# Kernel tuning notes

Measured on AMD Instinct MI355X. Metric: run time of the kernel, lower is better.

The kernel has to match this reference:

```python
import math
import jax, jax.numpy as jnp
import numpy as np

B, S, D = 4, 2048, 1024
EPS_LN = 1e-5
EPS_MAS = 1e-9


def layernorm(x, g, b):
    m = jnp.mean(x, axis=-1, keepdims=True)
    v = jnp.mean(jnp.square(x - m), axis=-1, keepdims=True)
    return (x - m) * jax.lax.rsqrt(v + EPS_LN) * g + b


def spl(x, proto_w, mu_w, mu_b, gate):
    # match_values = x @ proto^T / sqrt(d);  comp = silu(x @ mu^T + b)
    match = jnp.einsum('bsd,od->bso', x, proto_w) / math.sqrt(x.shape[-1])
    comp = jax.nn.silu(jnp.einsum('bsd,od->bso', x, mu_w) + mu_b)
    return comp, match, gate


def branch(comp, match, gate, passthrough):
    # mas_normalize on the 1-D gate vector (cost), broadcast over [B,S,D]
    cost = gate / (jnp.max(jnp.abs(gate)) + EPS_MAS)
    rl = match - cost
    mrl = jax.nn.relu(rl)
    mask = (rl > 0).astype(comp.dtype)
    return comp * mrl + passthrough * (1.0 - mask)


def causal_attention(q, k, v):
    # num_heads = 1, head_dim = D, is_causal=True
    scale = 1.0 / math.sqrt(q.shape[-1])
    scores = jnp.einsum('bqd,bkd->bqk', q, k) * scale
    causal = jnp.tril(jnp.ones((q.shape[1], k.shape[1]), dtype=bool))
    scores = jnp.where(causal, scores, jnp.asarray(-1e9, scores.dtype))
    p = jax.nn.softmax(scores, axis=-1)
    return jnp.einsum('bqk,bkd->bqd', p, v)


def setup_inputs() -> dict:
    key = jax.random.key(0)
    ks = jax.random.split(key, 16)
    d = D
    std = 0.02
    inp = {
        'x': jax.random.normal(ks[0], (B, S, d), jnp.float32),
        'ln_g': jnp.ones((d,), jnp.float32),
        'ln_b': jnp.zeros((d,), jnp.float32),
    }
    names = ['q', 'k', 'v', 'o']
    for i, n in enumerate(names):
        inp[f'{n}_mu_w'] = std * jax.random.normal(ks[1 + 3 * i], (d, d), jnp.float32)
        inp[f'{n}_mu_b'] = jnp.zeros((d,), jnp.float32)
        inp[f'{n}_proto'] = std * jax.random.normal(ks[2 + 3 * i], (d, d), jnp.float32)
        inp[f'{n}_gate'] = 0.1 * jax.random.normal(ks[3 + 3 * i], (d,), jnp.float32)
    return inp


def reference(x, ln_g, ln_b,
              q_mu_w, q_mu_b, q_proto, q_gate,
              k_mu_w, k_mu_b, k_proto, k_gate,
              v_mu_w, v_mu_b, v_proto, v_gate,
              o_mu_w, o_mu_b, o_proto, o_gate):
    ln1_out = layernorm(x, ln_g, ln_b)

    c_q, mv_q, g_q = spl(ln1_out, q_proto, q_mu_w, q_mu_b, q_gate)
    c_k, mv_k, g_k = spl(ln1_out, k_proto, k_mu_w, k_mu_b, k_gate)
    c_v, mv_v, g_v = spl(ln1_out, v_proto, v_mu_w, v_mu_b, v_gate)

    q = branch(c_q, mv_q, g_q, ln1_out)
    k = branch(c_k, mv_k, g_k, ln1_out)
    v = branch(c_v, mv_v, g_v, ln1_out)

    attn_out = causal_attention(q, k, v)

    c_o, mv_o, g_o = spl(attn_out, o_proto, o_mu_w, o_mu_b, o_gate)
    masked_o = branch(c_o, mv_o, g_o, attn_out)

    x_out = x + masked_o
    return x_out
```

## Files before the change

kernel.cpp:

```cpp
#include <hip/hip_runtime.h>
#include <hip/hip_bf16.h>
#include <cmath>
#include <cstdint>

typedef _Float16 f16;
typedef _Float16 f16x8 __attribute__((ext_vector_type(8)));
typedef float f32x4 __attribute__((ext_vector_type(4)));

#define D_ 1024
#define S_ 2048


__device__ __forceinline__ void gload_lds16(const void* g, void* l) {
  __builtin_amdgcn_global_load_lds(
      (const __attribute__((address_space(1))) void*)(unsigned long long)(uintptr_t)g,
      (__attribute__((address_space(3))) void*)(unsigned int)(uintptr_t)l,
      16, 0, 0);
}

__device__ __forceinline__ int lds_off(int row, int cb) {
  return (row << 5) + ((cb ^ ((row >> 1) & 3)) << 3);
}

__device__ __forceinline__ void split1024(float v, f16& h, f16& l) {
  float s = v * 1024.f;
  h = (f16)s;
  l = (f16)(s - (float)h);
}

__device__ __forceinline__ void stage_tile(const f16* __restrict__ src, int ld,
                                           f16* lds, int wid, int lane) {
  const int r = (wid << 5) + (lane >> 2);
  const int c = (lane & 3) ^ ((r >> 1) & 3);
  const f16* g0 = src + (size_t)r * ld + (c << 3);
  gload_lds16(g0, lds + (wid << 10));
  gload_lds16(g0 + (size_t)(ld << 4), lds + (wid << 10) + 512);
}

__global__ __launch_bounds__(256) void convert_w(
    const float* __restrict__ s0, const float* __restrict__ s1,
    const float* __restrict__ s2, const float* __restrict__ s3,
    const float* __restrict__ s4, const float* __restrict__ s5,
    const float* __restrict__ s6, const float* __restrict__ s7,
    f16* __restrict__ dst) {
  const float* srcs[8] = {s0, s1, s2, s3, s4, s5, s6, s7};
  const float* sp = srcs[blockIdx.y];
  f16* hi = dst + (size_t)blockIdx.y * 2097152;
  f16* lo = hi + 1048576;
  const int i = (blockIdx.x * 256 + threadIdx.x) << 2;
  float4 f = *(const float4*)(sp + i);
  __align__(8) f16 h4[4], l4[4];
  split1024(f.x, h4[0], l4[0]); split1024(f.y, h4[1], l4[1]);
  split1024(f.z, h4[2], l4[2]); split1024(f.w, h4[3], l4[3]);
  *(uint2*)(hi + i) = *(uint2*)h4;
  *(uint2*)(lo + i) = *(uint2*)l4;
}

__global__ __launch_bounds__(256) void cost_k(
    const float* __restrict__ g0, const float* __restrict__ g1,
    const float* __restrict__ g2, const float* __restrict__ g3,
    float* __restrict__ cost) {
  const float* gp = blockIdx.x == 0 ? g0 : blockIdx.x == 1 ? g1
                   : blockIdx.x == 2 ? g2 : g3;
  const int t = threadIdx.x;
  float4 v = *(const float4*)(gp + (t << 2));
  float mx = fmaxf(fmaxf(fabsf(v.x), fabsf(v.y)), fmaxf(fabsf(v.z), fabsf(v.w)));
  for (int o = 32; o; o >>= 1) mx = fmaxf(mx, __shfl_xor(mx, o, 64));
  __shared__ float red[4];
  if ((t & 63) == 0) red[t >> 6] = mx;
  __syncthreads();
  mx = fmaxf(fmaxf(red[0], red[1]), fmaxf(red[2], red[3]));
  const float den = mx + 1e-9f;
  float4 o = {v.x / den, v.y / den, v.z / den, v.w / den};
  *(float4*)(cost + (blockIdx.x << 10) + (t << 2)) = o;
}

__global__ __launch_bounds__(256) void layernorm_k(
    const float* __restrict__ x, const float* __restrict__ g,
    const float* __restrict__ bta, f16* __restrict__ Lh, f16* __restrict__ Ll) {
  const int row = blockIdx.x, t = threadIdx.x;
  const float* xr = x + (size_t)row * D_;
  float4 v = *(const float4*)(xr + (t << 2));
  float s = v.x + v.y + v.z + v.w;
  float q = v.x * v.x + v.y * v.y + v.z * v.z + v.w * v.w;
  for (int o = 32; o; o >>= 1) { s += __shfl_xor(s, o, 64); q += __shfl_xor(q, o, 64); }
  __shared__ float red[8];
  const int wid = t >> 6;
  if ((t & 63) == 0) { red[wid] = s; red[4 + wid] = q; }
  __syncthreads();
  s = red[0] + red[1] + red[2] + red[3];
  q = red[4] + red[5] + red[6] + red[7];
  const float mean = s * (1.f / D_);
  const float var = q * (1.f / D_) - mean * mean;
  const float inv = 1.f / sqrtf(var + 1e-5f);
  float4 gv = *(const float4*)(g + (t << 2));
  float4 bv = *(const float4*)(bta + (t << 2));
  __align__(8) f16 h4[4], l4[4];
  split1024((v.x - mean) * inv * gv.x + bv.x, h4[0], l4[0]);
  split1024((v.y - mean) * inv * gv.y + bv.y, h4[1], l4[1]);
  split1024((v.z - mean) * inv * gv.z + bv.z, h4[2], l4[2]);
  split1024((v.w - mean) * inv * gv.w + bv.w, h4[3], l4[3]);
  const size_t off = (size_t)row * D_ + (t << 2);
  *(uint2*)(Lh + off) = *(uint2*)h4;
  *(uint2*)(Ll + off) = *(uint2*)l4;
}

template <int EPI, int MUP>
__global__ __launch_bounds__(512, 1) void dual_gemm_v2(
    const f16* __restrict__ Ah, const f16* __restrict__ Al,
    const f16* __restrict__ Wph, const f16* __restrict__ Wpl,
    const f16* __restrict__ Wmh, const f16* __restrict__ Wml,
    const float* __restrict__ bias, const float* __restrict__ cost,
    const f16* __restrict__ passh, const f16* __restrict__ passl,
    const float* __restrict__ xres, f16* __restrict__ outh,
    f16* __restrict__ outl, float* __restrict__ outf) {
  __shared__ __align__(16) f16 smem[65536];
  const int tid = threadIdx.x, wid = tid >> 6, lane = tid & 63;
  const int row0 = blockIdx.x << 8, col0 = blockIdx.y << 7;
  const int wr = (wid >> 1) << 6, wc = (wid & 1) << 6;
  const int arow = lane & 15, cbk = lane >> 4;

  const int sr = tid >> 2;
  const int sc = ((tid & 3) ^ ((sr >> 1) & 3)) << 3;
  const int wbase = wid << 9;

  const f16* pA0 = Ah + (size_t)(row0 + sr) * D_ + sc;
  const f16* pA1 = Ah + (size_t)(row0 + 128 + sr) * D_ + sc;
  const f16* pL0 = Al + (size_t)(row0 + sr) * D_ + sc;
  const f16* pL1 = Al + (size_t)(row0 + 128 + sr) * D_ + sc;
  const f16* pPh = Wph + (size_t)(col0 + sr) * D_ + sc;
  const f16* pPl = Wpl + (size_t)(col0 + sr) * D_ + sc;
  const f16* pMh = Wmh + (size_t)(col0 + sr) * D_ + sc;
  const f16* pMl = Wml + (size_t)(col0 + sr) * D_ + sc;

  const f32x4 zero = {0.f, 0.f, 0.f, 0.f};
  f32x4 accP[4][4], accM[4][4];
#pragma unroll
  for (int m = 0; m < 4; ++m)
#pragma unroll
    for (int n = 0; n < 4; ++n) { accP[m][n] = zero; accM[m][n] = zero; }

  auto STAGE = [&](f16* buf, int k) {
    gload_lds16(pA0 + k, buf + wbase);
    gload_lds16(pA1 + k, buf + 4096 + wbase);
    gload_lds16(pL0 + k, buf + 8192 + wbase);
    gload_lds16(pL1 + k, buf + 12288 + wbase);
    gload_lds16(pPh + k, buf + 16384 + wbase);
    gload_lds16(pPl + k, buf + 20480 + wbase);
    gload_lds16(pMh + k, buf + 24576 + wbase);
    gload_lds16(pMl + k, buf + 28672 + wbase);
  };

  auto COMPUTE = [&](const f16* buf) {
    const f16* bAh = buf;
    const f16* bAl = buf + 8192;
    const f16* bPh = buf + 16384;
    const f16* bPl = buf + 20480;
    const f16* bMh = buf + 24576;
    const f16* bMl = buf + 28672;
    f16x8 ah[4], al[4];
#pragma unroll
    for (int m = 0; m < 4; ++m) {
      const int ao = lds_off(wr + m * 16 + arow, cbk);
      ah[m] = *(const f16x8*)&bAh[ao];
      al[m] = *(const f16x8*)&bAl[ao];
    }
#pragma unroll
    for (int n = 0; n < 4; ++n) {
      const int bo = lds_off(wc + n * 16 + arow, cbk);
      f16x8 bph = *(const f16x8*)&bPh[bo];
      f16x8 bpl = *(const f16x8*)&bPl[bo];
      f16x8 bmh = *(const f16x8*)&bMh[bo];
      f16x8 bml = *(const f16x8*)&bMl[bo];
#pragma unroll
      for (int m = 0; m < 4; ++m) {
        accP[m][n] = __builtin_amdgcn_mfma_f32_16x16x32_f16(ah[m], bph, accP[m][n], 0, 0, 0);
        accP[m][n] = __builtin_amdgcn_mfma_f32_16x16x32_f16(ah[m], bpl, accP[m][n], 0, 0, 0);
        accP[m][n] = __builtin_amdgcn_mfma_f32_16x16x32_f16(al[m], bph, accP[m][n], 0, 0, 0);
        accM[m][n] = __builtin_amdgcn_mfma_f32_16x16x32_f16(ah[m], bmh, accM[m][n], 0, 0, 0);
        accM[m][n] = __builtin_amdgcn_mfma_f32_16x16x32_f16(ah[m], bml, accM[m][n], 0, 0, 0);
        if (MUP == 3)
          accM[m][n] = __builtin_amdgcn_mfma_f32_16x16x32_f16(al[m], bmh, accM[m][n], 0, 0, 0);
      }
    }
  };

  STAGE(smem, 0);
  int cur = 0;
  for (int t = 0; t < 31; ++t) {
    STAGE(smem + ((cur ^ 1) << 15), (t + 1) << 5);
    asm volatile("s_waitcnt vmcnt(8)\n\ts_barrier" ::: "memory");
    __builtin_amdgcn_s_setprio(1);
    COMPUTE(smem + (cur << 15));
    __builtin_amdgcn_s_setprio(0);
    asm volatile("s_waitcnt lgkmcnt(0)\n\ts_barrier" ::: "memory");
    cur ^= 1;
  }
  asm volatile("s_waitcnt vmcnt(0)\n\ts_barrier" ::: "memory");
  __builtin_amdgcn_s_setprio(1);
  COMPUTE(smem + (cur << 15));
  __builtin_amdgcn_s_setprio(0);

#pragma unroll
  for (int m = 0; m < 4; ++m) {
    const int rb = row0 + wr + m * 16 + ((lane >> 4) << 2);
#pragma unroll
    for (int n = 0; n < 4; ++n) {
      const int col = col0 + wc + n * 16 + (lane & 15);
      const float cb2 = cost[col], bb = bias[col];
#pragma unroll
      for (int j = 0; j < 4; ++j) {
        const size_t off = (size_t)(rb + j) * D_ + col;
        const float match = accP[m][n][j] * (1.f / 33554432.f);
        const float pre = accM[m][n][j] * (1.f / 1048576.f) + bb;
        const float comp = pre / (1.f + expf(-pre));
        const float rl = match - cb2;
        float ov;
        if (rl > 0.f) ov = comp * rl;
        else ov = ((float)passh[off] + (float)passl[off]) * (1.f / 1024.f);
        if (EPI == 0) {
          f16 h, l; split1024(ov, h, l);
          outh[off] = h; outl[off] = l;
        } else {
          outf[off] = xres[off] + ov;
        }
      }
    }
  }
}

__global__ __launch_bounds__(256) void transpose_v(
    const f16* __restrict__ Vh, const f16* __restrict__ Vl,
    f16* __restrict__ VTh, f16* __restrict__ VTl) {
  const int iz = blockIdx.z, b = iz & 3;
  const f16* src = (iz >> 2) ? Vl : Vh;
  f16* dst = (iz >> 2) ? VTl : VTh;
  const int d0 = blockIdx.x << 6, s0 = blockIdx.y << 6;
  __shared__ f16 tl[64][65];
  const int c = threadIdx.x & 63, r4 = threadIdx.x >> 6;
  const f16* vb = src + (size_t)b * S_ * D_;
#pragma unroll
  for (int i = 0; i < 16; ++i) {
    const int sr = (r4 << 4) + i;
    tl[sr][c] = vb[(size_t)(s0 + sr) * D_ + d0 + c];
  }
  __syncthreads();
  f16* db = dst + (size_t)b * D_ * S_;
#pragma unroll
  for (int i = 0; i < 16; ++i) {
    const int dr = (r4 << 4) + i;
    db[(size_t)(d0 + dr) * S_ + s0 + c] = tl[c][dr];
  }
}

__global__ __launch_bounds__(256, 2) void scores_gemm(
    const f16* __restrict__ Qh, const f16* __restrict__ Ql,
    const f16* __restrict__ Kh, const f16* __restrict__ Kl,
    float* __restrict__ SC) {
  const int rt = blockIdx.x, ct = blockIdx.y, b = blockIdx.z;
  if (ct > rt) return;
  __shared__ __align__(16) f16 lQh[4096], lQl[4096], lKh[4096], lKl[4096];
  const int tid = threadIdx.x, wid = tid >> 6, lane = tid & 63;
  const int row0 = rt << 7, col0 = ct << 7;
  const int wr = (wid >> 1) << 6, wc = (wid & 1) << 6;
  const int arow = lane & 15, cb = lane >> 4;
  const f32x4 zero = {0.f, 0.f, 0.f, 0.f};
  f32x4 acc[4][4];
#pragma unroll
  for (int m = 0; m < 4; ++m)
#pragma unroll
    for (int n = 0; n < 4; ++n) acc[m][n] = zero;
  const f16* Qhb = Qh + ((size_t)b * S_ + row0) * D_;
  const f16* Qlb = Ql + ((size_t)b * S_ + row0) * D_;
  const f16* Khb = Kh + ((size_t)b * S_ + col0) * D_;
  const f16* Klb = Kl + ((size_t)b * S_ + col0) * D_;
  for (int k = 0; k < D_; k += 32) {
    stage_tile(Qhb + k, D_, lQh, wid, lane);
    stage_tile(Qlb + k, D_, lQl, wid, lane);
    stage_tile(Khb + k, D_, lKh, wid, lane);
    stage_tile(Klb + k, D_, lKl, wid, lane);
    __syncthreads();
    f16x8 bh[4], bl[4];
#pragma unroll
    for (int n = 0; n < 4; ++n) {
      const int bo = lds_off(wc + n * 16 + arow, cb);
      bh[n] = *(const f16x8*)&lKh[bo];
      bl[n] = *(const f16x8*)&lKl[bo];
    }
#pragma unroll
    for (int m = 0; m < 4; ++m) {
      const int ao = lds_off(wr + m * 16 + arow, cb);
      f16x8 ah = *(const f16x8*)&lQh[ao];
      f16x8 al = *(const f16x8*)&lQl[ao];
#pragma unroll
      for (int n = 0; n < 4; ++n) {
        acc[m][n] = __builtin_amdgcn_mfma_f32_16x16x32_f16(ah, bh[n], acc[m][n], 0, 0, 0);
        acc[m][n] = __builtin_amdgcn_mfma_f32_16x16x32_f16(ah, bl[n], acc[m][n], 0, 0, 0);
        acc[m][n] = __builtin_amdgcn_mfma_f32_16x16x32_f16(al, bh[n], acc[m][n], 0, 0, 0);
      }
    }
    __syncthreads();
  }
  float* scb = SC + (size_t)b * S_ * S_;
#pragma unroll
  for (int m = 0; m < 4; ++m) {
    const int rb = row0 + wr + m * 16 + ((lane >> 4) << 2);
#pragma unroll
    for (int n = 0; n < 4; ++n) {
      const int col = col0 + wc + n * 16 + (lane & 15);
#pragma unroll
      for (int j = 0; j < 4; ++j)
        scb[(size_t)(rb + j) * S_ + col] = acc[m][n][j] * (1.f / 33554432.f);
    }
  }
}

__global__ __launch_bounds__(256) void softmax_rows(float* __restrict__ SC) {
  const int r = blockIdx.x;
  const int s = r & 2047;
  float* rowf = SC + (size_t)r * S_;
  const int t = threadIdx.x, c0 = t << 3;
  float f[8];
  float4 u0 = *(const float4*)(rowf + c0);
  float4 u1 = *(const float4*)(rowf + c0 + 4);
  f[0] = u0.x; f[1] = u0.y; f[2] = u0.z; f[3] = u0.w;
  f[4] = u1.x; f[5] = u1.y; f[6] = u1.z; f[7] = u1.w;
  float mx = -3.0e38f;
#pragma unroll
  for (int j = 0; j < 8; ++j)
    if (c0 + j <= s) mx = fmaxf(mx, f[j]);
  for (int o = 32; o; o >>= 1) mx = fmaxf(mx, __shfl_xor(mx, o, 64));
  __shared__ float red[8];
  const int wid = t >> 6;
  if ((t & 63) == 0) red[wid] = mx;
  __syncthreads();
  mx = fmaxf(fmaxf(red[0], red[1]), fmaxf(red[2], red[3]));
  float e[8];
  float sum = 0.f;
#pragma unroll
  for (int j = 0; j < 8; ++j) {
    e[j] = (c0 + j <= s) ? expf(f[j] - mx) : 0.f;
    sum += e[j];
  }
  for (int o = 32; o; o >>= 1) sum += __shfl_xor(sum, o, 64);
  if ((t & 63) == 0) red[4 + wid] = sum;
  __syncthreads();
  sum = red[4] + red[5] + red[6] + red[7];
  f16* rowh = (f16*)rowf;
  __align__(16) f16 ph[8], pl[8];
#pragma unroll
  for (int j = 0; j < 8; ++j) {
    float p = (e[j] / sum) * 2048.f;
    ph[j] = (f16)p;
    pl[j] = (f16)(p - (float)ph[j]);
  }
  *(uint4*)(rowh + c0) = *(uint4*)ph;
  *(uint4*)(rowh + 2048 + c0) = *(uint4*)pl;
}

__global__ __launch_bounds__(256, 2) void pv_gemm(
    const f16* __restrict__ P, const f16* __restrict__ VTh,
    const f16* __restrict__ VTl, f16* __restrict__ Ath, f16* __restrict__ Atl) {
  const int rt = blockIdx.x, ct = blockIdx.y, b = blockIdx.z;
  __shared__ __align__(16) f16 lPh[4096], lPl[4096], lVh[4096], lVl[4096];
  const int tid = threadIdx.x, wid = tid >> 6, lane = tid & 63;
  const int row0 = rt << 7, col0 = ct << 7;
  const int wr = (wid >> 1) << 6, wc = (wid & 1) << 6;
  const int arow = lane & 15, cb = lane >> 4;
  const f32x4 zero = {0.f, 0.f, 0.f, 0.f};
  f32x4 acc[4][4];
#pragma unroll
  for (int m = 0; m < 4; ++m)
#pragma unroll
    for (int n = 0; n < 4; ++n) acc[m][n] = zero;
  const f16* Pb = P + ((size_t)b * S_ + row0) * 4096;
  const f16* Vhb = VTh + (size_t)b * D_ * S_ + (size_t)col0 * S_;
  const f16* Vlb = VTl + (size_t)b * D_ * S_ + (size_t)col0 * S_;
  const int kend = (rt + 1) << 7;
  for (int k = 0; k < kend; k += 32) {
    stage_tile(Pb + k, 4096, lPh, wid, lane);
    stage_tile(Pb + 2048 + k, 4096, lPl, wid, lane);
    stage_tile(Vhb + k, S_, lVh, wid, lane);
    stage_tile(Vlb + k, S_, lVl, wid, lane);
    __syncthreads();
    f16x8 bh[4], bl[4];
#pragma unroll
    for (int n = 0; n < 4; ++n) {
      const int bo = lds_off(wc + n * 16 + arow, cb);
      bh[n] = *(const f16x8*)&lVh[bo];
      bl[n] = *(const f16x8*)&lVl[bo];
    }
#pragma unroll
    for (int m = 0; m < 4; ++m) {
      const int ao = lds_off(wr + m * 16 + arow, cb);
      f16x8 ah = *(const f16x8*)&lPh[ao];
      f16x8 al = *(const f16x8*)&lPl[ao];
#pragma unroll
      for (int n = 0; n < 4; ++n) {
        acc[m][n] = __builtin_amdgcn_mfma_f32_16x16x32_f16(ah, bh[n], acc[m][n], 0, 0, 0);
        acc[m][n] = __builtin_amdgcn_mfma_f32_16x16x32_f16(ah, bl[n], acc[m][n], 0, 0, 0);
        acc[m][n] = __builtin_amdgcn_mfma_f32_16x16x32_f16(al, bh[n], acc[m][n], 0, 0, 0);
      }
    }
    __syncthreads();
  }
#pragma unroll
  for (int m = 0; m < 4; ++m) {
    const int rb = row0 + wr + m * 16 + ((lane >> 4) << 2);
#pragma unroll
    for (int n = 0; n < 4; ++n) {
      const int col = col0 + wc + n * 16 + (lane & 15);
#pragma unroll
      for (int j = 0; j < 4; ++j) {
        const float at = acc[m][n][j] * (1.f / 2097152.f);
        const size_t off = ((size_t)b * S_ + rb + j) * D_ + col;
        f16 h, l; split1024(at, h, l);
        Ath[off] = h; Atl[off] = l;
      }
    }
  }
}

extern "C" void kernel_launch(void* const* d_in, const int* in_sizes, int n_in,
                              void* d_out, int out_size, void* d_ws, size_t ws_size,
                              hipStream_t stream) {
  (void)in_sizes; (void)n_in; (void)out_size; (void)ws_size;
  const float* x      = (const float*)d_in[0];
  const float* ln_g   = (const float*)d_in[1];
  const float* ln_b   = (const float*)d_in[2];
  const float* q_mu_w = (const float*)d_in[3];
  const float* q_mu_b = (const float*)d_in[4];
  const float* q_pro  = (const float*)d_in[5];
  const float* q_gate = (const float*)d_in[6];
  const float* k_mu_w = (const float*)d_in[7];
  const float* k_mu_b = (const float*)d_in[8];
  const float* k_pro  = (const float*)d_in[9];
  const float* k_gate = (const float*)d_in[10];
  const float* v_mu_w = (const float*)d_in[11];
  const float* v_mu_b = (const float*)d_in[12];
  const float* v_pro  = (const float*)d_in[13];
  const float* v_gate = (const float*)d_in[14];
  const float* o_mu_w = (const float*)d_in[15];
  const float* o_mu_b = (const float*)d_in[16];
  const float* o_pro  = (const float*)d_in[17];
  const float* o_gate = (const float*)d_in[18];

  char* w = (char*)d_ws;
  f16* WB = (f16*)w;
  const size_t WS = 2097152;
  f16* Lh  = (f16*)(w + 33554432);
  f16* Ll  = (f16*)(w + 50331648);
  f16* Qh  = (f16*)(w + 67108864);
  f16* Ql  = (f16*)(w + 83886080);
  f16* Kh  = (f16*)(w + 100663296);
  f16* Kl  = (f16*)(w + 117440512);
  f16* VTh = (f16*)(w + 134217728);
  f16* VTl = (f16*)(w + 150994944);
  float* SC = (float*)(w + 167772160);
  float* COST = (float*)(w + 234881024);
  f16* Vh = (f16*)SC;
  f16* Vl = (f16*)(w + 184549376);
  f16* Ath = Qh;  f16* Atl = Ql;

  convert_w<<<dim3(1024, 8), 256, 0, stream>>>(
      q_pro, q_mu_w, k_pro, k_mu_w, v_pro, v_mu_w, o_pro, o_mu_w, WB);
  cost_k<<<4, 256, 0, stream>>>(q_gate, k_gate, v_gate, o_gate, COST);
  layernorm_k<<<8192, 256, 0, stream>>>(x, ln_g, ln_b, Lh, Ll);

  dual_gemm_v2<0, 3><<<dim3(32, 8), 512, 0, stream>>>(
      Lh, Ll, WB, WB + 1048576, WB + WS, WB + WS + 1048576,
      q_mu_b, COST, Lh, Ll, nullptr, Qh, Ql, nullptr);
  dual_gemm_v2<0, 3><<<dim3(32, 8), 512, 0, stream>>>(
      Lh, Ll, WB + 2 * WS, WB + 2 * WS + 1048576, WB + 3 * WS, WB + 3 * WS + 1048576,
      k_mu_b, COST + 1024, Lh, Ll, nullptr, Kh, Kl, nullptr);
  dual_gemm_v2<0, 3><<<dim3(32, 8), 512, 0, stream>>>(
      Lh, Ll, WB + 4 * WS, WB + 4 * WS + 1048576, WB + 5 * WS, WB + 5 * WS + 1048576,
      v_mu_b, COST + 2048, Lh, Ll, nullptr, Vh, Vl, nullptr);

  transpose_v<<<dim3(16, 32, 8), 256, 0, stream>>>(Vh, Vl, VTh, VTl);
  scores_gemm<<<dim3(16, 16, 4), 256, 0, stream>>>(Qh, Ql, Kh, Kl, SC);
  softmax_rows<<<8192, 256, 0, stream>>>(SC);
  pv_gemm<<<dim3(16, 8, 4), 256, 0, stream>>>((const f16*)SC, VTh, VTl, Ath, Atl);

  dual_gemm_v2<1, 2><<<dim3(32, 8), 512, 0, stream>>>(
      Ath, Atl, WB + 6 * WS, WB + 6 * WS + 1048576, WB + 7 * WS, WB + 7 * WS + 1048576,
      o_mu_b, COST + 3072, Ath, Atl, x, nullptr, nullptr, (float*)d_out);
}
```

Measured before the change: 712.3 us.

## Interleave next-tile global-to-LDS loads with MFMA phases in dual GEMM

The dual GEMM main loop now issues the next tile's global-to-LDS loads in pairs, spread across four per-column MFMA phases, instead of all eight loads up front. Each phase waits on its own LDS reads and ends with a barrier, and the LDS read offsets are hoisted out of the loop. The goal is to overlap memory traffic with matrix work and smooth out bursts of outstanding loads. In exchange there are more barriers per K step, and the last iteration issues a redundant reload of tile 0.

Result: faster. 678.9 us (-4.7%).

```diff
diff --git a/kernel.cpp b/kernel.cpp
--- a/kernel.cpp
+++ b/kernel.cpp
@@ -105,8 +105,35 @@
   *(uint2*)(Ll + off) = *(uint2*)l4;
 }
 
+#define MFMA16(a, b, c) __builtin_amdgcn_mfma_f32_16x16x32_f16((a), (b), (c), 0, 0, 0)
+
+#define PH_CORE(N)                                                        \
+    const f16x8 bph = *(const f16x8*)&bb[16384 + boff[N]];                \
+    const f16x8 bpl = *(const f16x8*)&bb[20480 + boff[N]];                \
+    const f16x8 bmh = *(const f16x8*)&bb[24576 + boff[N]];                \
+    const f16x8 bml = *(const f16x8*)&bb[28672 + boff[N]];                \
+    asm volatile("s_waitcnt lgkmcnt(0)" ::: "memory");                    \
+    __builtin_amdgcn_sched_barrier(0);                                    \
+    __builtin_amdgcn_s_setprio(1);                                        \
+    _Pragma("unroll")                                                     \
+    for (int m = 0; m < 4; ++m) {                                         \
+      accP[m][N] = MFMA16(ah[m], bph, accP[m][N]);                        \
+      accP[m][N] = MFMA16(ah[m], bpl, accP[m][N]);                        \
+      accP[m][N] = MFMA16(al[m], bph, accP[m][N]);                        \
+      accM[m][N] = MFMA16(ah[m], bmh, accM[m][N]);                        \
+      accM[m][N] = MFMA16(ah[m], bml, accM[m][N]);                        \
+      if (MUP == 3) accM[m][N] = MFMA16(al[m], bmh, accM[m][N]);          \
+    }                                                                     \
+    __builtin_amdgcn_s_setprio(0);                                        \
+    asm volatile("s_barrier" ::: "memory");
+
+#define DOPHASE_S(N, G0, L0, G1, L1)                                      \
+  { gload_lds16((G0), (L0)); gload_lds16((G1), (L1)); PH_CORE(N) }
+
+#define DOPHASE_N(N) { PH_CORE(N) }
+
 template <int EPI, int MUP>
-__global__ __launch_bounds__(512, 1) void dual_gemm_v2(
+__global__ __launch_bounds__(512, 1) void dual_gemm_v3(
     const f16* __restrict__ Ah, const f16* __restrict__ Al,
     const f16* __restrict__ Wph, const f16* __restrict__ Wpl,
     const f16* __restrict__ Wmh, const f16* __restrict__ Wml,
@@ -140,66 +167,42 @@
 #pragma unroll
     for (int n = 0; n < 4; ++n) { accP[m][n] = zero; accM[m][n] = zero; }
 
-  auto STAGE = [&](f16* buf, int k) {
-    gload_lds16(pA0 + k, buf + wbase);
-    gload_lds16(pA1 + k, buf + 4096 + wbase);
-    gload_lds16(pL0 + k, buf + 8192 + wbase);
-    gload_lds16(pL1 + k, buf + 12288 + wbase);
-    gload_lds16(pPh + k, buf + 16384 + wbase);
-    gload_lds16(pPl + k, buf + 20480 + wbase);
-    gload_lds16(pMh + k, buf + 24576 + wbase);
-    gload_lds16(pMl + k, buf + 28672 + wbase);
-  };
-
-  auto COMPUTE = [&](const f16* buf) {
-    const f16* bAh = buf;
-    const f16* bAl = buf + 8192;
-    const f16* bPh = buf + 16384;
-    const f16* bPl = buf + 20480;
-    const f16* bMh = buf + 24576;
-    const f16* bMl = buf + 28672;
+  int aoff[4], boff[4];
+#pragma unroll
+  for (int m = 0; m < 4; ++m) aoff[m] = lds_off(wr + m * 16 + arow, cbk);
+#pragma unroll
+  for (int n = 0; n < 4; ++n) boff[n] = lds_off(wc + n * 16 + arow, cbk);
+
+  {
+    f16* b = smem;
+    gload_lds16(pA0, b + wbase);          gload_lds16(pA1, b + 4096 + wbase);
+    gload_lds16(pL0, b + 8192 + wbase);   gload_lds16(pL1, b + 12288 + wbase);
+    gload_lds16(pPh, b + 16384 + wbase);  gload_lds16(pPl, b + 20480 + wbase);
+    gload_lds16(pMh, b + 24576 + wbase);  gload_lds16(pMl, b + 28672 + wbase);
+  }
+
+  int cur = 0;
+  for (int t = 0; t < 32; ++t) {
+    const f16* bb = smem + (cur << 15);
+    f16* nb = smem + ((cur ^ 1) << 15);
+    const int kn = (t < 31) ? ((t + 1) << 5) : 0;
+
     f16x8 ah[4], al[4];
+    gload_lds16(pA0 + kn, nb + wbase);
+    gload_lds16(pA1 + kn, nb + 4096 + wbase);
+    asm volatile("s_waitcnt vmcnt(2)\n\ts_barrier" ::: "memory");
+    __builtin_amdgcn_sched_barrier(0);
 #pragma unroll
     for (int m = 0; m < 4; ++m) {
-      const int ao = lds_off(wr + m * 16 + arow, cbk);
-      ah[m] = *(const f16x8*)&bAh[ao];
-      al[m] = *(const f16x8*)&bAl[ao];
-    }
-#pragma unroll
-    for (int n = 0; n < 4; ++n) {
-      const int bo = lds_off(wc + n * 16 + arow, cbk);
-      f16x8 bph = *(const f16x8*)&bPh[bo];
-      f16x8 bpl = *(const f16x8*)&bPl[bo];
-      f16x8 bmh = *(const f16x8*)&bMh[bo];
-      f16x8 bml = *(const f16x8*)&bMl[bo];
-#pragma unroll
-      for (int m = 0; m < 4; ++m) {
-        accP[m][n] = __builtin_amdgcn_mfma_f32_16x16x32_f16(ah[m], bph, accP[m][n], 0, 0, 0);
-        accP[m][n] = __builtin_amdgcn_mfma_f32_16x16x32_f16(ah[m], bpl, accP[m][n], 0, 0, 0);
-        accP[m][n] = __builtin_amdgcn_mfma_f32_16x16x32_f16(al[m], bph, accP[m][n], 0, 0, 0);
-        accM[m][n] = __builtin_amdgcn_mfma_f32_16x16x32_f16(ah[m], bmh, accM[m][n], 0, 0, 0);
-        accM[m][n] = __builtin_amdgcn_mfma_f32_16x16x32_f16(ah[m], bml, accM[m][n], 0, 0, 0);
-        if (MUP == 3)
-          accM[m][n] = __builtin_amdgcn_mfma_f32_16x16x32_f16(al[m], bmh, accM[m][n], 0, 0, 0);
-      }
-    }
-  };
-
-  STAGE(smem, 0);
-  int cur = 0;
-  for (int t = 0; t < 31; ++t) {
-    STAGE(smem + ((cur ^ 1) << 15), (t + 1) << 5);
-    asm volatile("s_waitcnt vmcnt(8)\n\ts_barrier" ::: "memory");
-    __builtin_amdgcn_s_setprio(1);
-    COMPUTE(smem + (cur << 15));
-    __builtin_amdgcn_s_setprio(0);
-    asm volatile("s_waitcnt lgkmcnt(0)\n\ts_barrier" ::: "memory");
+      ah[m] = *(const f16x8*)&bb[aoff[m]];
+      al[m] = *(const f16x8*)&bb[8192 + aoff[m]];
+    }
+    DOPHASE_S(0, pL0 + kn, nb + 8192 + wbase, pL1 + kn, nb + 12288 + wbase)
+    DOPHASE_S(1, pPh + kn, nb + 16384 + wbase, pPl + kn, nb + 20480 + wbase)
+    DOPHASE_S(2, pMh + kn, nb + 24576 + wbase, pMl + kn, nb + 28672 + wbase)
+    DOPHASE_N(3)
     cur ^= 1;
   }
-  asm volatile("s_waitcnt vmcnt(0)\n\ts_barrier" ::: "memory");
-  __builtin_amdgcn_s_setprio(1);
-  COMPUTE(smem + (cur << 15));
-  __builtin_amdgcn_s_setprio(0);
 
 #pragma unroll
   for (int m = 0; m < 4; ++m) {
@@ -207,12 +210,12 @@
 #pragma unroll
     for (int n = 0; n < 4; ++n) {
       const int col = col0 + wc + n * 16 + (lane & 15);
-      const float cb2 = cost[col], bb = bias[col];
+      const float cb2 = cost[col], bbv = bias[col];
 #pragma unroll
       for (int j = 0; j < 4; ++j) {
         const size_t off = (size_t)(rb + j) * D_ + col;
         const float match = accP[m][n][j] * (1.f / 33554432.f);
-        const float pre = accM[m][n][j] * (1.f / 1048576.f) + bb;
+        const float pre = accM[m][n][j] * (1.f / 1048576.f) + bbv;
         const float comp = pre / (1.f + expf(-pre));
         const float rl = match - cb2;
         float ov;
@@ -467,13 +470,13 @@
   cost_k<<<4, 256, 0, stream>>>(q_gate, k_gate, v_gate, o_gate, COST);
   layernorm_k<<<8192, 256, 0, stream>>>(x, ln_g, ln_b, Lh, Ll);
 
-  dual_gemm_v2<0, 3><<<dim3(32, 8), 512, 0, stream>>>(
+  dual_gemm_v3<0, 3><<<dim3(32, 8), 512, 0, stream>>>(
       Lh, Ll, WB, WB + 1048576, WB + WS, WB + WS + 1048576,
       q_mu_b, COST, Lh, Ll, nullptr, Qh, Ql, nullptr);
-  dual_gemm_v2<0, 3><<<dim3(32, 8), 512, 0, stream>>>(
+  dual_gemm_v3<0, 3><<<dim3(32, 8), 512, 0, stream>>>(
       Lh, Ll, WB + 2 * WS, WB + 2 * WS + 1048576, WB + 3 * WS, WB + 3 * WS + 1048576,
       k_mu_b, COST + 1024, Lh, Ll, nullptr, Kh, Kl, nullptr);
-  dual_gemm_v2<0, 3><<<dim3(32, 8), 512, 0, stream>>>(
+  dual_gemm_v3<0, 3><<<dim3(32, 8), 512, 0, stream>>>(
       Lh, Ll, WB + 4 * WS, WB + 4 * WS + 1048576, WB + 5 * WS, WB + 5 * WS + 1048576,
       v_mu_b, COST + 2048, Lh, Ll, nullptr, Vh, Vl, nullptr);
 
@@ -482,7 +485,7 @@
   softmax_rows<<<8192, 256, 0, stream>>>(SC);
   pv_gemm<<<dim3(16, 8, 4), 256, 0, stream>>>((const f16*)SC, VTh, VTl, Ath, Atl);
 
-  dual_gemm_v2<1, 2><<<dim3(32, 8), 512, 0, stream>>>(
+  dual_gemm_v3<1, 2><<<dim3(32, 8), 512, 0, stream>>>(
       Ath, Atl, WB + 6 * WS, WB + 6 * WS + 1048576, WB + 7 * WS, WB + 7 * WS + 1048576,
       o_mu_b, COST + 3072, Ath, Atl, x, nullptr, nullptr, (float*)d_out);
 }
```
